# Kernel optimization log

Measured on AMD Instinct MI355X. Metric: run time of the kernel, lower is better.

Reference implementation:

```python
import jax, jax.numpy as jnp
import numpy as np

TEMPERATURE = 0.5


def setup_inputs() -> dict:
    key = jax.random.key(0)
    k1, k2 = jax.random.split(key)
    emb = jax.random.normal(k1, (16384, 128), dtype=jnp.float32)
    emb = emb / jnp.linalg.norm(emb, axis=1, keepdims=True)  # L2-normalized, per docstring
    labels = jax.random.randint(k2, (16384,), 0, 64, dtype=jnp.int64)
    return {"embeddings": emb, "partition_labels": labels}


def reference(embeddings, partition_labels):
    n = embeddings.shape[0]
    # [N, N] similarity matrix, scaled by temperature
    sim = jnp.matmul(embeddings, embeddings.T) / TEMPERATURE
    exp_sim = jnp.exp(sim)
    eye = jnp.eye(n, dtype=bool)
    pos_mask = (partition_labels[None, :] == partition_labels[:, None]) & ~eye
    # numerator: sum of exp over positives; denominator: sum over all k != i
    pos_sum = jnp.sum(jnp.where(pos_mask, exp_sim, 0.0), axis=1)
    all_sum = jnp.sum(jnp.where(~eye, exp_sim, 0.0), axis=1)
    valid = jnp.any(pos_mask, axis=1)
    loss_i = -(jnp.log(pos_sum) - jnp.log(all_sum))
    n_valid = jnp.sum(valid)
    total = jnp.sum(jnp.where(valid, loss_i, 0.0))
    return jnp.where(n_valid > 0, total / n_valid, 0.0)
```

## Files before the change

### kernel.cpp

```cpp
#include <hip/hip_runtime.h>

#define N_EMB 16384
#define DIM 128
#define NSPLIT 16
#define CPS (N_EMB / NSPLIT)
#define BN 128
#define NCT (CPS / BN)
#define NLAB 64

typedef __bf16 bf16x8 __attribute__((ext_vector_type(8)));
typedef float f32x4 __attribute__((ext_vector_type(4)));
typedef unsigned short us8 __attribute__((ext_vector_type(8)));
typedef unsigned int u32;

#define SCALE 2.8853900817779268f
#define LN2 0.6931471805599453f

__device__ inline float fast_exp2(float x) {
#if __has_builtin(__builtin_amdgcn_exp2f)
  return __builtin_amdgcn_exp2f(x);
#else
  return exp2f(x);
#endif
}
__device__ inline float fast_log2(float x) {
#if __has_builtin(__builtin_amdgcn_logf)
  return __builtin_amdgcn_logf(x);
#else
  return log2f(x);
#endif
}

__device__ inline unsigned short f2bf(float f) {
  unsigned int u = __float_as_uint(f);
  u += 0x7fffu + ((u >> 16) & 1u);
  return (unsigned short)(u >> 16);
}

__device__ inline void gll16(const unsigned short* g, unsigned short* l) {
  __builtin_amdgcn_global_load_lds(
      (const __attribute__((address_space(1))) u32*)g,
      (__attribute__((address_space(3))) u32*)l, 16, 0, 0);
}

__global__ __launch_bounds__(1024) void perm_kernel(
    const int* __restrict__ labels, int* __restrict__ perm,
    int* __restrict__ gstart) {
  __shared__ int whist[16][NLAB];
  __shared__ int htot[NLAB];
  const int tid = threadIdx.x;
  const int w = tid >> 6, lane = tid & 63;
  whist[w][lane] = 0;
  __syncthreads();
  const int base_i = w * 1024;
  int mylab[16];
#pragma unroll
  for (int k = 0; k < 16; ++k) {
    int lab = labels[base_i + k * 64 + lane];
    mylab[k] = lab;
    atomicAdd(&whist[w][lab], 1);
  }
  __syncthreads();
  if (tid < NLAB) {
    int s = 0;
#pragma unroll
    for (int ww = 0; ww < 16; ++ww) {
      int t = whist[ww][tid];
      whist[ww][tid] = s;
      s += t;
    }
    htot[tid] = s;
  }
  __syncthreads();
  if (tid == 0) {
    int s = 0;
    for (int l = 0; l < NLAB; ++l) {
      int t = htot[l];
      gstart[l] = s;
      htot[l] = s;
      s += t;
    }
    gstart[NLAB] = s;
  }
  __syncthreads();
  whist[w][lane] += htot[lane];
  __syncthreads();
#pragma unroll
  for (int k = 0; k < 16; ++k) {
    int lab = mylab[k];
    int pos = atomicAdd(&whist[w][lab], 1);
    perm[pos] = base_i + k * 64 + lane;
  }
}

__global__ __launch_bounds__(256) void preconv(
    const float* __restrict__ emb, const int* __restrict__ perm,
    unsigned short* __restrict__ eraw) {
  const int tid = threadIdx.x;
  const int tile = blockIdx.x >> 2;
  const int part = blockIdx.x & 3;
  const size_t base = (size_t)tile * (128 * DIM);
#pragma unroll
  for (int i = 0; i < 2; ++i) {
    int G = part * 512 + i * 256 + tid;
    int col16 = G & 15;
    int qd = (G >> 4) & 3;
    int ks = (G >> 6) & 3;
    int tc = G >> 8;
    int srow = perm[tile * 128 + tc * 16 + col16];
    const float* p = emb + (size_t)srow * DIM + ks * 32 + qd * 8;
    float4 a = *reinterpret_cast<const float4*>(p);
    float4 b = *reinterpret_cast<const float4*>(p + 4);
    us8 g;
    g[0] = f2bf(a.x); g[1] = f2bf(a.y); g[2] = f2bf(a.z); g[3] = f2bf(a.w);
    g[4] = f2bf(b.x); g[5] = f2bf(b.y); g[6] = f2bf(b.z); g[7] = f2bf(b.w);
    *reinterpret_cast<us8*>(eraw + base + (size_t)G * 8) = g;
  }
}

__device__ inline bf16x8 load_scaled(const unsigned short* p) {
  us8 v = *reinterpret_cast<const us8*>(p);
  us8 s;
#pragma unroll
  for (int j = 0; j < 8; ++j)
    s[j] = f2bf(__uint_as_float((u32)v[j] << 16) * SCALE);
  return *reinterpret_cast<bf16x8*>(&s);
}

__global__ __launch_bounds__(256) void cl_all(
    const unsigned short* __restrict__ eraw, float* __restrict__ ws_all) {
  __shared__ unsigned short lds[BN * DIM];
  const int tid = threadIdx.x;
  const int lane = tid & 63;
  const int w = tid >> 6;
  const int col16 = lane & 15;
  const int quad = lane >> 4;
  const int r0 = blockIdx.x * 256;
  const int cs = blockIdx.y;

  bf16x8 afrag[4][4];
#pragma unroll
  for (int tr = 0; tr < 4; ++tr) {
    const int T = (r0 >> 4) + w * 4 + tr;
    const unsigned short* p = eraw + (size_t)(T >> 3) * (128 * DIM) +
                              ((T & 7) * 4) * 512 + lane * 8;
#pragma unroll
    for (int ks = 0; ks < 4; ++ks) afrag[tr][ks] = load_scaled(p + ks * 512);
  }

  float all_p[16];
#pragma unroll
  for (int t = 0; t < 16; ++t) all_p[t] = 0.f;

  for (int ct = 0; ct < NCT; ++ct) {
    const int c0 = cs * CPS + ct * BN;
    __syncthreads();
    {
      const unsigned short* g = eraw + (size_t)c0 * DIM;
#pragma unroll
      for (int i = 0; i < 8; ++i) {
        int chunk = i * 4 + w;
        gll16(g + chunk * 512 + lane * 8, lds + chunk * 512);
      }
    }
    __syncthreads();

#pragma unroll
    for (int tc = 0; tc < 8; ++tc) {
      bf16x8 bfr[4];
#pragma unroll
      for (int ks = 0; ks < 4; ++ks)
        bfr[ks] = *reinterpret_cast<const bf16x8*>(lds + (tc * 4 + ks) * 512 +
                                                   lane * 8);
#pragma unroll
      for (int tr = 0; tr < 4; ++tr) {
        f32x4 acc = {0.f, 0.f, 0.f, 0.f};
#pragma unroll
        for (int ks = 0; ks < 4; ++ks)
          acc = __builtin_amdgcn_mfma_f32_16x16x32_bf16(afrag[tr][ks], bfr[ks],
                                                        acc, 0, 0, 0);
#pragma unroll
        for (int r = 0; r < 4; ++r) all_p[tr * 4 + r] += fast_exp2(acc[r]);
      }
    }
  }

#pragma unroll
  for (int t = 0; t < 16; ++t) {
    float a = all_p[t];
#pragma unroll
    for (int m = 8; m >= 1; m >>= 1) a += __shfl_xor(a, m, 64);
    if (col16 == 0) {
      int row_g = r0 + w * 64 + (t >> 2) * 16 + quad * 4 + (t & 3);
      ws_all[cs * N_EMB + row_g] = a;
    }
  }
}

__global__ __launch_bounds__(256) void cl_pos(
    const unsigned short* __restrict__ eraw, const int* __restrict__ gstart,
    float* __restrict__ ws_pos, float* __restrict__ ws_diag) {
  const int l = blockIdx.x;
  const int chunk = blockIdx.y;
  const int gs = gstart[l], ge = gstart[l + 1];
  const int tid = threadIdx.x;
  const int lane = tid & 63;
  const int w = tid >> 6;
  const int col16 = lane & 15;
  const int quad = lane >> 4;
  const int t0 = gs >> 4;
  const int t1 = (ge + 15) >> 4;

  for (int ta = t0 + chunk * 4 + w; ta < t1; ta += 16) {
    bf16x8 af[4];
    const unsigned short* pa = eraw + (size_t)(ta >> 3) * (128 * DIM) +
                               ((ta & 7) * 4) * 512 + lane * 8;
#pragma unroll
    for (int ks = 0; ks < 4; ++ks) af[ks] = load_scaled(pa + ks * 512);
    const int grow = ta * 16 + quad * 4;
    float posr[4] = {0.f, 0.f, 0.f, 0.f};

    for (int tb = t0; tb < t1; ++tb) {
      bf16x8 bfr[4];
      const unsigned short* pb = eraw + (size_t)(tb >> 3) * (128 * DIM) +
                                 ((tb & 7) * 4) * 512 + lane * 8;
#pragma unroll
      for (int ks = 0; ks < 4; ++ks)
        bfr[ks] = *reinterpret_cast<const bf16x8*>(pb + ks * 512);
      f32x4 acc = {0.f, 0.f, 0.f, 0.f};
#pragma unroll
      for (int ks = 0; ks < 4; ++ks)
        acc = __builtin_amdgcn_mfma_f32_16x16x32_bf16(af[ks], bfr[ks], acc, 0,
                                                      0, 0);
      const int gcol = tb * 16 + col16;
      const bool colin = (gcol >= gs) && (gcol < ge);
#pragma unroll
      for (int r = 0; r < 4; ++r) {
        float e = fast_exp2(acc[r]);
        const int gr = grow + r;
        if (gcol == gr) {
          if (colin) ws_diag[gr] = e;
        } else if (colin) {
          posr[r] += e;
        }
      }
    }

#pragma unroll
    for (int r = 0; r < 4; ++r) {
      float p = posr[r];
#pragma unroll
      for (int m = 8; m >= 1; m >>= 1) p += __shfl_xor(p, m, 64);
      const int gr = grow + r;
      if (col16 == 0 && gr >= gs && gr < ge) ws_pos[gr] = p;
    }
  }
}

__global__ __launch_bounds__(256) void fin1(
    const float* __restrict__ ws_all, const float* __restrict__ ws_pos,
    const float* __restrict__ ws_diag, float* __restrict__ part_tot,
    int* __restrict__ part_cnt) {
  __shared__ float s_t[256];
  __shared__ int s_c[256];
  const int tid = threadIdx.x;
  const int row = blockIdx.x * 256 + tid;
  float a = 0.f;
#pragma unroll
  for (int s = 0; s < NSPLIT; ++s) a += ws_all[s * N_EMB + row];
  a -= ws_diag[row];
  const float p = ws_pos[row];
  float t = 0.f;
  int c = 0;
  if (p > 0.f) {
    t = fast_log2(a) - fast_log2(p);
    c = 1;
  }
  s_t[tid] = t;
  s_c[tid] = c;
  __syncthreads();
  for (int s = 128; s > 0; s >>= 1) {
    if (tid < s) {
      s_t[tid] += s_t[tid + s];
      s_c[tid] += s_c[tid + s];
    }
    __syncthreads();
  }
  if (tid == 0) {
    part_tot[blockIdx.x] = s_t[0];
    part_cnt[blockIdx.x] = s_c[0];
  }
}

__global__ __launch_bounds__(64) void fin2(const float* __restrict__ part_tot,
                                           const int* __restrict__ part_cnt,
                                           float* __restrict__ out) {
  const int tid = threadIdx.x;
  float t = part_tot[tid];
  int c = part_cnt[tid];
#pragma unroll
  for (int m = 32; m >= 1; m >>= 1) {
    t += __shfl_xor(t, m, 64);
    c += __shfl_xor(c, m, 64);
  }
  if (tid == 0) out[0] = (c > 0) ? (t * LN2 / (float)c) : 0.f;
}

extern "C" void kernel_launch(void* const* d_in, const int* in_sizes, int n_in,
                              void* d_out, int out_size, void* d_ws,
                              size_t ws_size, hipStream_t stream) {
  const float* emb = (const float*)d_in[0];
  const int* labels = (const int*)d_in[1];

  unsigned short* eraw = (unsigned short*)d_ws;
  float* ws_all = (float*)(eraw + (size_t)N_EMB * DIM);
  float* ws_pos = ws_all + NSPLIT * N_EMB;
  float* ws_diag = ws_pos + N_EMB;
  float* part_tot = ws_diag + N_EMB;
  int* part_cnt = (int*)(part_tot + 64);
  int* perm = part_cnt + 64;
  int* gstart = perm + N_EMB;

  perm_kernel<<<1, 1024, 0, stream>>>(labels, perm, gstart);
  preconv<<<512, 256, 0, stream>>>(emb, perm, eraw);
  cl_all<<<dim3(N_EMB / 256, NSPLIT), 256, 0, stream>>>(eraw, ws_all);
  cl_pos<<<dim3(NLAB, 4), 256, 0, stream>>>(eraw, gstart, ws_pos, ws_diag);
  fin1<<<N_EMB / 256, 256, 0, stream>>>(ws_all, ws_pos, ws_diag, part_tot,
                                        part_cnt);
  fin2<<<1, 64, 0, stream>>>(part_tot, part_cnt, (float*)d_out);
}
```

Before: 166.1 us.

## Fuse all-sum and positive-sum kernels with double-buffered LDS staging

```diff
diff --git a/kernel.cpp b/kernel.cpp
--- a/kernel.cpp
+++ b/kernel.cpp
@@ -4,9 +4,10 @@
 #define DIM 128
 #define NSPLIT 16
 #define CPS (N_EMB / NSPLIT)
-#define BN 128
+#define BN 64
 #define NCT (CPS / BN)
 #define NLAB 64
+#define POSY 4
 
 typedef __bf16 bf16x8 __attribute__((ext_vector_type(8)));
 typedef float f32x4 __attribute__((ext_vector_type(4)));
@@ -127,132 +128,138 @@
   return *reinterpret_cast<bf16x8*>(&s);
 }
 
-__global__ __launch_bounds__(256) void cl_all(
-    const unsigned short* __restrict__ eraw, float* __restrict__ ws_all) {
-  __shared__ unsigned short lds[BN * DIM];
+__global__ __launch_bounds__(128) void cl_fused(
+    const unsigned short* __restrict__ eraw, const int* __restrict__ gstart,
+    float* __restrict__ ws_all, float* __restrict__ ws_pos,
+    float* __restrict__ ws_diag) {
+  __shared__ unsigned short lds0[BN * DIM];
+  __shared__ unsigned short lds1[BN * DIM];
   const int tid = threadIdx.x;
   const int lane = tid & 63;
   const int w = tid >> 6;
   const int col16 = lane & 15;
   const int quad = lane >> 4;
-  const int r0 = blockIdx.x * 256;
   const int cs = blockIdx.y;
 
-  bf16x8 afrag[4][4];
-#pragma unroll
-  for (int tr = 0; tr < 4; ++tr) {
-    const int T = (r0 >> 4) + w * 4 + tr;
-    const unsigned short* p = eraw + (size_t)(T >> 3) * (128 * DIM) +
-                              ((T & 7) * 4) * 512 + lane * 8;
-#pragma unroll
-    for (int ks = 0; ks < 4; ++ks) afrag[tr][ks] = load_scaled(p + ks * 512);
-  }
-
-  float all_p[16];
-#pragma unroll
-  for (int t = 0; t < 16; ++t) all_p[t] = 0.f;
-
-  for (int ct = 0; ct < NCT; ++ct) {
-    const int c0 = cs * CPS + ct * BN;
+  if (cs < NSPLIT) {
+    const int r0 = blockIdx.x * 128;
+
+    bf16x8 afrag[4][4];
+#pragma unroll
+    for (int tr = 0; tr < 4; ++tr) {
+      const int T = (r0 >> 4) + w * 4 + tr;
+      const unsigned short* p = eraw + (size_t)(T >> 3) * (128 * DIM) +
+                                ((T & 7) * 4) * 512 + lane * 8;
+#pragma unroll
+      for (int ks = 0; ks < 4; ++ks) afrag[tr][ks] = load_scaled(p + ks * 512);
+    }
+
+    float all_p[16];
+#pragma unroll
+    for (int t = 0; t < 16; ++t) all_p[t] = 0.f;
+
+    auto stage = [&](unsigned short* dst, int c0) {
+      const unsigned short* g = eraw + (size_t)(c0 >> 7) * (128 * DIM) +
+                                (size_t)((c0 >> 6) & 1) * 8192;
+#pragma unroll
+      for (int i = 0; i < 8; ++i) {
+        int chunk = i * 2 + w;
+        gll16(g + chunk * 512 + lane * 8, dst + chunk * 512);
+      }
+    };
+    auto computeB = [&](const unsigned short* buf) {
+#pragma unroll
+      for (int tc = 0; tc < 4; ++tc) {
+        bf16x8 bfr[4];
+#pragma unroll
+        for (int ks = 0; ks < 4; ++ks)
+          bfr[ks] = *reinterpret_cast<const bf16x8*>(buf + (tc * 4 + ks) * 512 +
+                                                     lane * 8);
+#pragma unroll
+        for (int tr = 0; tr < 4; ++tr) {
+          f32x4 acc = {0.f, 0.f, 0.f, 0.f};
+#pragma unroll
+          for (int ks = 0; ks < 4; ++ks)
+            acc = __builtin_amdgcn_mfma_f32_16x16x32_bf16(afrag[tr][ks],
+                                                          bfr[ks], acc, 0, 0, 0);
+#pragma unroll
+          for (int r = 0; r < 4; ++r) all_p[tr * 4 + r] += fast_exp2(acc[r]);
+        }
+      }
+    };
+
+    const int cbase = cs * CPS;
+    stage(lds0, cbase);
     __syncthreads();
-    {
-      const unsigned short* g = eraw + (size_t)c0 * DIM;
-#pragma unroll
-      for (int i = 0; i < 8; ++i) {
-        int chunk = i * 4 + w;
-        gll16(g + chunk * 512 + lane * 8, lds + chunk * 512);
-      }
-    }
-    __syncthreads();
-
-#pragma unroll
-    for (int tc = 0; tc < 8; ++tc) {
-      bf16x8 bfr[4];
-#pragma unroll
-      for (int ks = 0; ks < 4; ++ks)
-        bfr[ks] = *reinterpret_cast<const bf16x8*>(lds + (tc * 4 + ks) * 512 +
-                                                   lane * 8);
-#pragma unroll
-      for (int tr = 0; tr < 4; ++tr) {
+    for (int ct = 0; ct < NCT; ct += 2) {
+      if (ct + 1 < NCT) stage(lds1, cbase + (ct + 1) * BN);
+      computeB(lds0);
+      __syncthreads();
+      if (ct + 2 < NCT) stage(lds0, cbase + (ct + 2) * BN);
+      computeB(lds1);
+      __syncthreads();
+    }
+
+#pragma unroll
+    for (int t = 0; t < 16; ++t) {
+      float a = all_p[t];
+#pragma unroll
+      for (int m = 8; m >= 1; m >>= 1) a += __shfl_xor(a, m, 64);
+      if (col16 == 0) {
+        int row_g = r0 + w * 64 + (t >> 2) * 16 + quad * 4 + (t & 3);
+        ws_all[cs * N_EMB + row_g] = a;
+      }
+    }
+  } else {
+    const int l = blockIdx.x >> 1;
+    const int chunk = (cs - NSPLIT) * 2 + (blockIdx.x & 1);
+    const int gs = gstart[l], ge = gstart[l + 1];
+    const int t0 = gs >> 4;
+    const int t1 = (ge + 15) >> 4;
+
+    for (int ta = t0 + chunk * 2 + w; ta < t1; ta += 16) {
+      bf16x8 af[4];
+      const unsigned short* pa = eraw + (size_t)(ta >> 3) * (128 * DIM) +
+                                 ((ta & 7) * 4) * 512 + lane * 8;
+#pragma unroll
+      for (int ks = 0; ks < 4; ++ks) af[ks] = load_scaled(pa + ks * 512);
+      const int grow = ta * 16 + quad * 4;
+      float posr[4] = {0.f, 0.f, 0.f, 0.f};
+
+      for (int tb = t0; tb < t1; ++tb) {
+        bf16x8 bfr[4];
+        const unsigned short* pb = eraw + (size_t)(tb >> 3) * (128 * DIM) +
+                                   ((tb & 7) * 4) * 512 + lane * 8;
+#pragma unroll
+        for (int ks = 0; ks < 4; ++ks)
+          bfr[ks] = *reinterpret_cast<const bf16x8*>(pb + ks * 512);
         f32x4 acc = {0.f, 0.f, 0.f, 0.f};
 #pragma unroll
         for (int ks = 0; ks < 4; ++ks)
-          acc = __builtin_amdgcn_mfma_f32_16x16x32_bf16(afrag[tr][ks], bfr[ks],
-                                                        acc, 0, 0, 0);
-#pragma unroll
-        for (int r = 0; r < 4; ++r) all_p[tr * 4 + r] += fast_exp2(acc[r]);
-      }
-    }
-  }
-
-#pragma unroll
-  for (int t = 0; t < 16; ++t) {
-    float a = all_p[t];
-#pragma unroll
-    for (int m = 8; m >= 1; m >>= 1) a += __shfl_xor(a, m, 64);
-    if (col16 == 0) {
-      int row_g = r0 + w * 64 + (t >> 2) * 16 + quad * 4 + (t & 3);
-      ws_all[cs * N_EMB + row_g] = a;
-    }
-  }
-}
-
-__global__ __launch_bounds__(256) void cl_pos(
-    const unsigned short* __restrict__ eraw, const int* __restrict__ gstart,
-    float* __restrict__ ws_pos, float* __restrict__ ws_diag) {
-  const int l = blockIdx.x;
-  const int chunk = blockIdx.y;
-  const int gs = gstart[l], ge = gstart[l + 1];
-  const int tid = threadIdx.x;
-  const int lane = tid & 63;
-  const int w = tid >> 6;
-  const int col16 = lane & 15;
-  const int quad = lane >> 4;
-  const int t0 = gs >> 4;
-  const int t1 = (ge + 15) >> 4;
-
-  for (int ta = t0 + chunk * 4 + w; ta < t1; ta += 16) {
-    bf16x8 af[4];
-    const unsigned short* pa = eraw + (size_t)(ta >> 3) * (128 * DIM) +
-                               ((ta & 7) * 4) * 512 + lane * 8;
-#pragma unroll
-    for (int ks = 0; ks < 4; ++ks) af[ks] = load_scaled(pa + ks * 512);
-    const int grow = ta * 16 + quad * 4;
-    float posr[4] = {0.f, 0.f, 0.f, 0.f};
-
-    for (int tb = t0; tb < t1; ++tb) {
-      bf16x8 bfr[4];
-      const unsigned short* pb = eraw + (size_t)(tb >> 3) * (128 * DIM) +
-                                 ((tb & 7) * 4) * 512 + lane * 8;
-#pragma unroll
-      for (int ks = 0; ks < 4; ++ks)
-        bfr[ks] = *reinterpret_cast<const bf16x8*>(pb + ks * 512);
-      f32x4 acc = {0.f, 0.f, 0.f, 0.f};
-#pragma unroll
-      for (int ks = 0; ks < 4; ++ks)
-        acc = __builtin_amdgcn_mfma_f32_16x16x32_bf16(af[ks], bfr[ks], acc, 0,
-                                                      0, 0);
-      const int gcol = tb * 16 + col16;
-      const bool colin = (gcol >= gs) && (gcol < ge);
+          acc = __builtin_amdgcn_mfma_f32_16x16x32_bf16(af[ks], bfr[ks], acc,
+                                                        0, 0, 0);
+        const int gcol = tb * 16 + col16;
+        const bool colin = (gcol >= gs) && (gcol < ge);
+#pragma unroll
+        for (int r = 0; r < 4; ++r) {
+          float e = fast_exp2(acc[r]);
+          const int gr = grow + r;
+          if (gcol == gr) {
+            if (colin) ws_diag[gr] = e;
+          } else if (colin) {
+            posr[r] += e;
+          }
+        }
+      }
+
 #pragma unroll
       for (int r = 0; r < 4; ++r) {
-        float e = fast_exp2(acc[r]);
+        float p = posr[r];
+#pragma unroll
+        for (int m = 8; m >= 1; m >>= 1) p += __shfl_xor(p, m, 64);
         const int gr = grow + r;
-        if (gcol == gr) {
-          if (colin) ws_diag[gr] = e;
-        } else if (colin) {
-          posr[r] += e;
-        }
-      }
-    }
-
-#pragma unroll
-    for (int r = 0; r < 4; ++r) {
-      float p = posr[r];
-#pragma unroll
-      for (int m = 8; m >= 1; m >>= 1) p += __shfl_xor(p, m, 64);
-      const int gr = grow + r;
-      if (col16 == 0 && gr >= gs && gr < ge) ws_pos[gr] = p;
+        if (col16 == 0 && gr >= gs && gr < ge) ws_pos[gr] = p;
+      }
     }
   }
 }
@@ -323,8 +330,8 @@
 
   perm_kernel<<<1, 1024, 0, stream>>>(labels, perm, gstart);
   preconv<<<512, 256, 0, stream>>>(emb, perm, eraw);
-  cl_all<<<dim3(N_EMB / 256, NSPLIT), 256, 0, stream>>>(eraw, ws_all);
-  cl_pos<<<dim3(NLAB, 4), 256, 0, stream>>>(eraw, gstart, ws_pos, ws_diag);
+  cl_fused<<<dim3(128, NSPLIT + POSY), 128, 0, stream>>>(eraw, gstart, ws_all,
+                                                         ws_pos, ws_diag);
   fin1<<<N_EMB / 256, 256, 0, stream>>>(ws_all, ws_pos, ws_diag, part_tot,
                                         part_cnt);
   fin2<<<1, 64, 0, stream>>>(part_tot, part_cnt, (float*)d_out);
```

Measured after the change: 155.9 us. -6.2%, faster.

## Fuse perm and conversion into one prep kernel, merge all-sum and positive-sum kernels

Applied to the files above, without the earlier changes.

```diff
diff --git a/kernel.cpp b/kernel.cpp
--- a/kernel.cpp
+++ b/kernel.cpp
@@ -7,6 +7,7 @@
 #define BN 128
 #define NCT (CPS / BN)
 #define NLAB 64
+#define POSY 4
 
 typedef __bf16 bf16x8 __attribute__((ext_vector_type(8)));
 typedef float f32x4 __attribute__((ext_vector_type(4)));
@@ -43,78 +44,71 @@
       (__attribute__((address_space(3))) u32*)l, 16, 0, 0);
 }
 
-__global__ __launch_bounds__(1024) void perm_kernel(
-    const int* __restrict__ labels, int* __restrict__ perm,
+__global__ __launch_bounds__(256) void prep(
+    const float* __restrict__ emb, const int* __restrict__ labels,
+    unsigned short* __restrict__ eraw, int* __restrict__ perm,
     int* __restrict__ gstart) {
-  __shared__ int whist[16][NLAB];
-  __shared__ int htot[NLAB];
-  const int tid = threadIdx.x;
-  const int w = tid >> 6, lane = tid & 63;
-  whist[w][lane] = 0;
-  __syncthreads();
-  const int base_i = w * 1024;
-  int mylab[16];
-#pragma unroll
-  for (int k = 0; k < 16; ++k) {
-    int lab = labels[base_i + k * 64 + lane];
-    mylab[k] = lab;
-    atomicAdd(&whist[w][lab], 1);
-  }
-  __syncthreads();
-  if (tid < NLAB) {
-    int s = 0;
-#pragma unroll
-    for (int ww = 0; ww < 16; ++ww) {
-      int t = whist[ww][tid];
-      whist[ww][tid] = s;
-      s += t;
-    }
-    htot[tid] = s;
-  }
-  __syncthreads();
-  if (tid == 0) {
-    int s = 0;
-    for (int l = 0; l < NLAB; ++l) {
-      int t = htot[l];
-      gstart[l] = s;
-      htot[l] = s;
-      s += t;
-    }
-    gstart[NLAB] = s;
-  }
-  __syncthreads();
-  whist[w][lane] += htot[lane];
-  __syncthreads();
-#pragma unroll
-  for (int k = 0; k < 16; ++k) {
-    int lab = mylab[k];
-    int pos = atomicAdd(&whist[w][lab], 1);
-    perm[pos] = base_i + k * 64 + lane;
-  }
-}
-
-__global__ __launch_bounds__(256) void preconv(
-    const float* __restrict__ emb, const int* __restrict__ perm,
-    unsigned short* __restrict__ eraw) {
-  const int tid = threadIdx.x;
-  const int tile = blockIdx.x >> 2;
-  const int part = blockIdx.x & 3;
-  const size_t base = (size_t)tile * (128 * DIM);
-#pragma unroll
-  for (int i = 0; i < 2; ++i) {
-    int G = part * 512 + i * 256 + tid;
-    int col16 = G & 15;
-    int qd = (G >> 4) & 3;
-    int ks = (G >> 6) & 3;
-    int tc = G >> 8;
-    int srow = perm[tile * 128 + tc * 16 + col16];
-    const float* p = emb + (size_t)srow * DIM + ks * 32 + qd * 8;
-    float4 a = *reinterpret_cast<const float4*>(p);
-    float4 b = *reinterpret_cast<const float4*>(p + 4);
-    us8 g;
-    g[0] = f2bf(a.x); g[1] = f2bf(a.y); g[2] = f2bf(a.z); g[3] = f2bf(a.w);
-    g[4] = f2bf(b.x); g[5] = f2bf(b.y); g[6] = f2bf(b.z); g[7] = f2bf(b.w);
-    *reinterpret_cast<us8*>(eraw + base + (size_t)G * 8) = g;
+  if (blockIdx.x < 512) {
+    const int tid = threadIdx.x;
+    const int tile = blockIdx.x >> 2;
+    const int part = blockIdx.x & 3;
+    const size_t base = (size_t)tile * (128 * DIM);
+#pragma unroll
+    for (int i = 0; i < 2; ++i) {
+      int G = part * 512 + i * 256 + tid;
+      int col16 = G & 15;
+      int qd = (G >> 4) & 3;
+      int ks = (G >> 6) & 3;
+      int tc = G >> 8;
+      int srow = tile * 128 + tc * 16 + col16;
+      const float* p = emb + (size_t)srow * DIM + ks * 32 + qd * 8;
+      float4 a = *reinterpret_cast<const float4*>(p);
+      float4 b = *reinterpret_cast<const float4*>(p + 4);
+      us8 g;
+      g[0] = f2bf(a.x); g[1] = f2bf(a.y); g[2] = f2bf(a.z); g[3] = f2bf(a.w);
+      g[4] = f2bf(b.x); g[5] = f2bf(b.y); g[6] = f2bf(b.z); g[7] = f2bf(b.w);
+      *reinterpret_cast<us8*>(eraw + base + (size_t)G * 8) = g;
+    }
+  } else {
+    __shared__ int whist[4][NLAB];
+    __shared__ int htot[NLAB];
+    const int tid = threadIdx.x;
+    const int w = tid >> 6, lane = tid & 63;
+    whist[w][lane] = 0;
+    __syncthreads();
+    const int base_i = w * 4096;
+    for (int k = 0; k < 64; ++k)
+      atomicAdd(&whist[w][labels[base_i + k * 64 + lane]], 1);
+    __syncthreads();
+    if (tid < NLAB) {
+      int s = 0;
+#pragma unroll
+      for (int ww = 0; ww < 4; ++ww) {
+        int t = whist[ww][tid];
+        whist[ww][tid] = s;
+        s += t;
+      }
+      htot[tid] = s;
+    }
+    __syncthreads();
+    if (tid == 0) {
+      int s = 0;
+      for (int l = 0; l < NLAB; ++l) {
+        int t = htot[l];
+        gstart[l] = s;
+        htot[l] = s;
+        s += t;
+      }
+      gstart[NLAB] = s;
+    }
+    __syncthreads();
+    whist[w][lane] += htot[lane];
+    __syncthreads();
+    for (int k = 0; k < 64; ++k) {
+      int row = base_i + k * 64 + lane;
+      int pos = atomicAdd(&whist[w][labels[row]], 1);
+      perm[pos] = row;
+    }
   }
 }
 
@@ -127,147 +121,156 @@
   return *reinterpret_cast<bf16x8*>(&s);
 }
 
-__global__ __launch_bounds__(256) void cl_all(
-    const unsigned short* __restrict__ eraw, float* __restrict__ ws_all) {
+__device__ inline const unsigned short* frag_ptr(
+    const unsigned short* __restrict__ eraw, int r, int quad, int ks) {
+  return eraw + (size_t)(r >> 7) * (128 * DIM) +
+         (size_t)((((r >> 4) & 7) * 4 + ks) * 512 + (quad * 16 + (r & 15)) * 8);
+}
+
+__global__ __launch_bounds__(128) void cl_fused(
+    const unsigned short* __restrict__ eraw, const int* __restrict__ perm,
+    const int* __restrict__ gstart, float* __restrict__ ws_all,
+    float* __restrict__ ws_pos, float* __restrict__ ws_diag) {
   __shared__ unsigned short lds[BN * DIM];
   const int tid = threadIdx.x;
   const int lane = tid & 63;
   const int w = tid >> 6;
   const int col16 = lane & 15;
   const int quad = lane >> 4;
-  const int r0 = blockIdx.x * 256;
-  const int cs = blockIdx.y;
-
-  bf16x8 afrag[4][4];
-#pragma unroll
-  for (int tr = 0; tr < 4; ++tr) {
-    const int T = (r0 >> 4) + w * 4 + tr;
-    const unsigned short* p = eraw + (size_t)(T >> 3) * (128 * DIM) +
-                              ((T & 7) * 4) * 512 + lane * 8;
-#pragma unroll
-    for (int ks = 0; ks < 4; ++ks) afrag[tr][ks] = load_scaled(p + ks * 512);
-  }
-
-  float all_p[16];
-#pragma unroll
-  for (int t = 0; t < 16; ++t) all_p[t] = 0.f;
-
-  for (int ct = 0; ct < NCT; ++ct) {
-    const int c0 = cs * CPS + ct * BN;
-    __syncthreads();
-    {
-      const unsigned short* g = eraw + (size_t)c0 * DIM;
-#pragma unroll
-      for (int i = 0; i < 8; ++i) {
-        int chunk = i * 4 + w;
-        gll16(g + chunk * 512 + lane * 8, lds + chunk * 512);
-      }
-    }
-    __syncthreads();
-
-#pragma unroll
-    for (int tc = 0; tc < 8; ++tc) {
-      bf16x8 bfr[4];
+
+  if (blockIdx.y >= POSY) {
+    const int cs = blockIdx.y - POSY;
+    const int r0 = blockIdx.x * 128;
+
+    bf16x8 afrag[4][4];
+#pragma unroll
+    for (int tr = 0; tr < 4; ++tr) {
+      const int T = (r0 >> 4) + w * 4 + tr;
+      const unsigned short* p = eraw + (size_t)(T >> 3) * (128 * DIM) +
+                                ((T & 7) * 4) * 512 + lane * 8;
+#pragma unroll
+      for (int ks = 0; ks < 4; ++ks) afrag[tr][ks] = load_scaled(p + ks * 512);
+    }
+
+    float all_p[16];
+#pragma unroll
+    for (int t = 0; t < 16; ++t) all_p[t] = 0.f;
+
+    for (int ct = 0; ct < NCT; ++ct) {
+      __syncthreads();
+      {
+        const unsigned short* g =
+            eraw + (size_t)(cs * NCT + ct) * (128 * DIM);
+#pragma unroll
+        for (int i = 0; i < 16; ++i) {
+          int chunk = i * 2 + w;
+          gll16(g + chunk * 512 + lane * 8, lds + chunk * 512);
+        }
+      }
+      __syncthreads();
+
+#pragma unroll
+      for (int tc = 0; tc < 8; ++tc) {
+        bf16x8 bfr[4];
+#pragma unroll
+        for (int ks = 0; ks < 4; ++ks)
+          bfr[ks] = *reinterpret_cast<const bf16x8*>(lds + (tc * 4 + ks) * 512 +
+                                                     lane * 8);
+#pragma unroll
+        for (int tr = 0; tr < 4; ++tr) {
+          f32x4 acc = {0.f, 0.f, 0.f, 0.f};
+#pragma unroll
+          for (int ks = 0; ks < 4; ++ks)
+            acc = __builtin_amdgcn_mfma_f32_16x16x32_bf16(afrag[tr][ks],
+                                                          bfr[ks], acc, 0, 0,
+                                                          0);
+#pragma unroll
+          for (int r = 0; r < 4; ++r) all_p[tr * 4 + r] += fast_exp2(acc[r]);
+        }
+      }
+    }
+
+#pragma unroll
+    for (int t = 0; t < 16; ++t) {
+      float a = all_p[t];
+#pragma unroll
+      for (int m = 8; m >= 1; m >>= 1) a += __shfl_xor(a, m, 64);
+      if (col16 == 0) {
+        int row_g = r0 + w * 64 + (t >> 2) * 16 + quad * 4 + (t & 3);
+        ws_all[(size_t)row_g * NSPLIT + cs] = a;
+      }
+    }
+  } else {
+    const int l = blockIdx.x >> 1;
+    const int chunk = blockIdx.y * 2 + (blockIdx.x & 1);
+    const int gs = gstart[l], ge = gstart[l + 1];
+    const int rows = ge - gs;
+    const int nt = (rows + 15) >> 4;
+
+    for (int ti = chunk * 2 + w; ti < nt; ti += 16) {
+      const int ga = gs + ti * 16 + col16;
+      const int ra = (ga < ge) ? perm[ga] : perm[gs];
+      bf16x8 af[4];
 #pragma unroll
       for (int ks = 0; ks < 4; ++ks)
-        bfr[ks] = *reinterpret_cast<const bf16x8*>(lds + (tc * 4 + ks) * 512 +
-                                                   lane * 8);
-#pragma unroll
-      for (int tr = 0; tr < 4; ++tr) {
+        af[ks] = load_scaled(frag_ptr(eraw, ra, quad, ks));
+      const int grow_l = ti * 16 + quad * 4;
+      float posr[4] = {0.f, 0.f, 0.f, 0.f};
+
+      for (int tj = 0; tj < nt; ++tj) {
+        const int gb = gs + tj * 16 + col16;
+        const int rb = (gb < ge) ? perm[gb] : perm[gs];
+        bf16x8 bfr[4];
+#pragma unroll
+        for (int ks = 0; ks < 4; ++ks)
+          bfr[ks] = *reinterpret_cast<const bf16x8*>(
+              frag_ptr(eraw, rb, quad, ks));
         f32x4 acc = {0.f, 0.f, 0.f, 0.f};
 #pragma unroll
         for (int ks = 0; ks < 4; ++ks)
-          acc = __builtin_amdgcn_mfma_f32_16x16x32_bf16(afrag[tr][ks], bfr[ks],
-                                                        acc, 0, 0, 0);
-#pragma unroll
-        for (int r = 0; r < 4; ++r) all_p[tr * 4 + r] += fast_exp2(acc[r]);
-      }
-    }
-  }
-
-#pragma unroll
-  for (int t = 0; t < 16; ++t) {
-    float a = all_p[t];
-#pragma unroll
-    for (int m = 8; m >= 1; m >>= 1) a += __shfl_xor(a, m, 64);
-    if (col16 == 0) {
-      int row_g = r0 + w * 64 + (t >> 2) * 16 + quad * 4 + (t & 3);
-      ws_all[cs * N_EMB + row_g] = a;
-    }
-  }
-}
-
-__global__ __launch_bounds__(256) void cl_pos(
-    const unsigned short* __restrict__ eraw, const int* __restrict__ gstart,
-    float* __restrict__ ws_pos, float* __restrict__ ws_diag) {
-  const int l = blockIdx.x;
-  const int chunk = blockIdx.y;
-  const int gs = gstart[l], ge = gstart[l + 1];
-  const int tid = threadIdx.x;
-  const int lane = tid & 63;
-  const int w = tid >> 6;
-  const int col16 = lane & 15;
-  const int quad = lane >> 4;
-  const int t0 = gs >> 4;
-  const int t1 = (ge + 15) >> 4;
-
-  for (int ta = t0 + chunk * 4 + w; ta < t1; ta += 16) {
-    bf16x8 af[4];
-    const unsigned short* pa = eraw + (size_t)(ta >> 3) * (128 * DIM) +
-                               ((ta & 7) * 4) * 512 + lane * 8;
-#pragma unroll
-    for (int ks = 0; ks < 4; ++ks) af[ks] = load_scaled(pa + ks * 512);
-    const int grow = ta * 16 + quad * 4;
-    float posr[4] = {0.f, 0.f, 0.f, 0.f};
-
-    for (int tb = t0; tb < t1; ++tb) {
-      bf16x8 bfr[4];
-      const unsigned short* pb = eraw + (size_t)(tb >> 3) * (128 * DIM) +
-                                 ((tb & 7) * 4) * 512 + lane * 8;
-#pragma unroll
-      for (int ks = 0; ks < 4; ++ks)
-        bfr[ks] = *reinterpret_cast<const bf16x8*>(pb + ks * 512);
-      f32x4 acc = {0.f, 0.f, 0.f, 0.f};
-#pragma unroll
-      for (int ks = 0; ks < 4; ++ks)
-        acc = __builtin_amdgcn_mfma_f32_16x16x32_bf16(af[ks], bfr[ks], acc, 0,
-                                                      0, 0);
-      const int gcol = tb * 16 + col16;
-      const bool colin = (gcol >= gs) && (gcol < ge);
+          acc = __builtin_amdgcn_mfma_f32_16x16x32_bf16(af[ks], bfr[ks], acc,
+                                                        0, 0, 0);
+        const int gcol_l = tj * 16 + col16;
+        const bool colin = gcol_l < rows;
+#pragma unroll
+        for (int r = 0; r < 4; ++r) {
+          float e = fast_exp2(acc[r]);
+          const int i_l = grow_l + r;
+          if (gcol_l == i_l) {
+            if (colin) ws_diag[perm[gs + i_l]] = e;
+          } else if (colin) {
+            posr[r] += e;
+          }
+        }
+      }
+
 #pragma unroll
       for (int r = 0; r < 4; ++r) {
-        float e = fast_exp2(acc[r]);
-        const int gr = grow + r;
-        if (gcol == gr) {
-          if (colin) ws_diag[gr] = e;
-        } else if (colin) {
-          posr[r] += e;
-        }
-      }
-    }
-
-#pragma unroll
-    for (int r = 0; r < 4; ++r) {
-      float p = posr[r];
-#pragma unroll
-      for (int m = 8; m >= 1; m >>= 1) p += __shfl_xor(p, m, 64);
-      const int gr = grow + r;
-      if (col16 == 0 && gr >= gs && gr < ge) ws_pos[gr] = p;
-    }
-  }
-}
-
-__global__ __launch_bounds__(256) void fin1(
+        float p = posr[r];
+#pragma unroll
+        for (int m = 8; m >= 1; m >>= 1) p += __shfl_xor(p, m, 64);
+        const int i_l = grow_l + r;
+        if (col16 == 0 && i_l < rows) ws_pos[perm[gs + i_l]] = p;
+      }
+    }
+  }
+}
+
+__global__ __launch_bounds__(1024) void fin1(
     const float* __restrict__ ws_all, const float* __restrict__ ws_pos,
     const float* __restrict__ ws_diag, float* __restrict__ part_tot,
     int* __restrict__ part_cnt) {
-  __shared__ float s_t[256];
-  __shared__ int s_c[256];
+  __shared__ float s_t[1024];
+  __shared__ int s_c[1024];
   const int tid = threadIdx.x;
-  const int row = blockIdx.x * 256 + tid;
+  const int row = blockIdx.x * 1024 + tid;
+  const float4* pa = reinterpret_cast<const float4*>(ws_all + (size_t)row * NSPLIT);
   float a = 0.f;
 #pragma unroll
-  for (int s = 0; s < NSPLIT; ++s) a += ws_all[s * N_EMB + row];
+  for (int q = 0; q < NSPLIT / 4; ++q) {
+    float4 v = pa[q];
+    a += v.x + v.y + v.z + v.w;
+  }
   a -= ws_diag[row];
   const float p = ws_pos[row];
   float t = 0.f;
@@ -279,7 +282,7 @@
   s_t[tid] = t;
   s_c[tid] = c;
   __syncthreads();
-  for (int s = 128; s > 0; s >>= 1) {
+  for (int s = 512; s > 0; s >>= 1) {
     if (tid < s) {
       s_t[tid] += s_t[tid + s];
       s_c[tid] += s_c[tid + s];
@@ -296,10 +299,10 @@
                                            const int* __restrict__ part_cnt,
                                            float* __restrict__ out) {
   const int tid = threadIdx.x;
-  float t = part_tot[tid];
-  int c = part_cnt[tid];
-#pragma unroll
-  for (int m = 32; m >= 1; m >>= 1) {
+  float t = (tid < 16) ? part_tot[tid] : 0.f;
+  int c = (tid < 16) ? part_cnt[tid] : 0;
+#pragma unroll
+  for (int m = 8; m >= 1; m >>= 1) {
     t += __shfl_xor(t, m, 64);
     c += __shfl_xor(c, m, 64);
   }
@@ -314,18 +317,17 @@
 
   unsigned short* eraw = (unsigned short*)d_ws;
   float* ws_all = (float*)(eraw + (size_t)N_EMB * DIM);
-  float* ws_pos = ws_all + NSPLIT * N_EMB;
+  float* ws_pos = ws_all + (size_t)N_EMB * NSPLIT;
   float* ws_diag = ws_pos + N_EMB;
   float* part_tot = ws_diag + N_EMB;
-  int* part_cnt = (int*)(part_tot + 64);
-  int* perm = part_cnt + 64;
+  int* part_cnt = (int*)(part_tot + 16);
+  int* perm = part_cnt + 16;
   int* gstart = perm + N_EMB;
 
-  perm_kernel<<<1, 1024, 0, stream>>>(labels, perm, gstart);
-  preconv<<<512, 256, 0, stream>>>(emb, perm, eraw);
-  cl_all<<<dim3(N_EMB / 256, NSPLIT), 256, 0, stream>>>(eraw, ws_all);
-  cl_pos<<<dim3(NLAB, 4), 256, 0, stream>>>(eraw, gstart, ws_pos, ws_diag);
-  fin1<<<N_EMB / 256, 256, 0, stream>>>(ws_all, ws_pos, ws_diag, part_tot,
-                                        part_cnt);
+  prep<<<513, 256, 0, stream>>>(emb, labels, eraw, perm, gstart);
+  cl_fused<<<dim3(128, POSY + NSPLIT), 128, 0, stream>>>(eraw, perm, gstart,
+                                                         ws_all, ws_pos,
+                                                         ws_diag);
+  fin1<<<16, 1024, 0, stream>>>(ws_all, ws_pos, ws_diag, part_tot, part_cnt);
   fin2<<<1, 64, 0, stream>>>(part_tot, part_cnt, (float*)d_out);
 }
```

Measured after the change: 184.9 us. 11.3% more time.
